# Optimization experiments

Measured on AMD Instinct MI355X. Metric: run time of the kernel, lower is better.

## Reference

```python
import jax, jax.numpy as jnp
import numpy as np

B, S, D, H, HD = 1, 4096, 1024, 16, 64
ROPE_THETA = 10000.0


def setup_inputs() -> dict:
    key = jax.random.key(0)
    ks = jax.random.split(key, 10)
    sc = 0.02
    hidden_states = jax.random.normal(ks[0], (B, S, D), dtype=jnp.float32)
    # sorted continuous timestamps in [0, S) (irregularly sampled time series)
    timestamps = jnp.sort(jax.random.uniform(ks[1], (B, S), dtype=jnp.float32), axis=-1) * S
    Wq = jax.random.normal(ks[2], (D, D), dtype=jnp.float32) * sc
    bq = jax.random.normal(ks[3], (D,), dtype=jnp.float32) * sc
    Wk = jax.random.normal(ks[4], (D, D), dtype=jnp.float32) * sc
    bk = jax.random.normal(ks[5], (D,), dtype=jnp.float32) * sc
    Wv = jax.random.normal(ks[6], (D, D), dtype=jnp.float32) * sc
    bv = jax.random.normal(ks[7], (D,), dtype=jnp.float32) * sc
    Wo = jax.random.normal(ks[8], (D, D), dtype=jnp.float32) * sc
    return dict(hidden_states=hidden_states, timestamps=timestamps,
                Wq=Wq, bq=bq, Wk=Wk, bk=bk, Wv=Wv, bv=bv, Wo=Wo)


def _rotate_half(x):
    x1, x2 = jnp.split(x, 2, axis=-1)
    return jnp.concatenate([-x2, x1], axis=-1)


def _ct_rope(q, k, timestamps):
    # q,k: [b,h,s,hd]; timestamps: [b,s] continuous positions
    inv_freq = 1.0 / (ROPE_THETA ** (jnp.arange(0, HD, 2, dtype=jnp.float32) / HD))
    angles = timestamps[:, None, :, None] * inv_freq  # [b,1,s,hd/2]
    angles = jnp.concatenate([angles, angles], axis=-1)  # [b,1,s,hd]
    cos, sin = jnp.cos(angles), jnp.sin(angles)
    q = q * cos + _rotate_half(q) * sin
    k = k * cos + _rotate_half(k) * sin
    return q, k


def reference(hidden_states, timestamps, Wq, bq, Wk, bk, Wv, bv, Wo):
    b, s, _ = hidden_states.shape
    # nn.Linear convention: y = x @ W.T + b
    q = (hidden_states @ Wq.T + bq).reshape(b, s, H, HD).transpose(0, 2, 1, 3)
    k = (hidden_states @ Wk.T + bk).reshape(b, s, H, HD).transpose(0, 2, 1, 3)
    v = (hidden_states @ Wv.T + bv).reshape(b, s, H, HD).transpose(0, 2, 1, 3)
    q, k = _ct_rope(q, k, timestamps)
    scores = jnp.einsum('bhqd,bhkd->bhqk', q, k) / jnp.sqrt(jnp.float32(HD))
    # causal additive mask (built as in HF Qwen2Model)
    causal = jnp.tril(jnp.ones((s, s), dtype=bool))
    neg = jnp.finfo(jnp.float32).min
    scores = jnp.where(causal[None, None], scores, neg)
    attn = jax.nn.softmax(scores.astype(jnp.float32), axis=-1).astype(q.dtype)
    out = jnp.einsum('bhqk,bhkd->bhqd', attn, v)
    out = out.transpose(0, 2, 1, 3).reshape(b, s, H * HD)
    return out @ Wo.T
```

## Files before the change

kernel.cpp:

```cpp
#include <hip/hip_runtime.h>

#define S_LEN  4096
#define DMODEL 1024
#define NHEAD  16
#define HDIM   64

typedef float    f32x4  __attribute__((ext_vector_type(4)));
typedef float    f32x16 __attribute__((ext_vector_type(16)));
typedef _Float16 f16x8  __attribute__((ext_vector_type(8)));
typedef _Float16 f16x4v __attribute__((ext_vector_type(4)));
typedef __fp16   fp16x2 __attribute__((ext_vector_type(2)));
typedef unsigned int u32;
typedef u32 u32x4 __attribute__((ext_vector_type(4)));

__device__ __forceinline__ void gl2lds16(const _Float16* g, _Float16* l) {
  __builtin_amdgcn_global_load_lds(
      (const __attribute__((address_space(1))) unsigned int*)g,
      (__attribute__((address_space(3))) unsigned int*)l, 16, 0, 0);
}

__device__ __forceinline__ u32 pkrtz_u(float a, float b) {
  fp16x2 h = __builtin_amdgcn_cvt_pkrtz(a, b);
  return __builtin_bit_cast(u32, h);
}

__device__ __forceinline__ float m3(float a, float b, float c) {
  return fmaxf(fmaxf(a, b), c);
}

__global__ void cast_f32_f16_k(const float* __restrict__ in,
                               _Float16* __restrict__ out, int n) {
  int i = (blockIdx.x * blockDim.x + threadIdx.x) * 4;
  if (i + 3 < n) {
    const float4 v = *(const float4*)(in + i);
    f16x4v o = { (_Float16)v.x, (_Float16)v.y, (_Float16)v.z, (_Float16)v.w };
    *(f16x4v*)(out + i) = o;
  }
}

__global__ void cast4_k(const float* __restrict__ a, const float* __restrict__ b,
                        const float* __restrict__ c, const float* __restrict__ d,
                        _Float16* __restrict__ oa, _Float16* __restrict__ ob,
                        _Float16* __restrict__ oc, _Float16* __restrict__ od) {
  const int seg = blockIdx.y;
  const float* in = seg == 0 ? a : seg == 1 ? b : seg == 2 ? c : d;
  _Float16*   out = seg == 0 ? oa : seg == 1 ? ob : seg == 2 ? oc : od;
  const int i = (blockIdx.x * blockDim.x + threadIdx.x) * 4;
  const float4 v = *(const float4*)(in + i);
  f16x4v o = { (_Float16)v.x, (_Float16)v.y, (_Float16)v.z, (_Float16)v.w };
  *(f16x4v*)(out + i) = o;
}

__global__ __launch_bounds__(256)
void gemm_qkv(const _Float16* __restrict__ A,
              const _Float16* __restrict__ Bw,
              const float* __restrict__ bq,
              const float* __restrict__ bk,
              const float* __restrict__ bv,
              const float* __restrict__ ts,
              _Float16* __restrict__ Qb,
              _Float16* __restrict__ Kb,
              _Float16* __restrict__ Vtb)
{
  __shared__ _Float16 lA[128 * 64];
  __shared__ _Float16 lB[128 * 64];

  const int tid  = threadIdx.x;
  const int wid  = tid >> 6;
  const int lane = tid & 63;
  const int l16  = lane & 15;
  const int lg   = lane >> 4;
  const int wr = wid >> 1, wc = wid & 1;
  const int m0 = blockIdx.y * 128, n0 = blockIdx.x * 128;
  const int K = DMODEL, M = S_LEN;

  const int lrow   = lane >> 3;
  const int gchunk = (lane & 7) ^ lrow;

  f32x4 acc[4][4] = {};

  for (int k0 = 0; k0 < K; k0 += 64) {
#pragma unroll
    for (int it = 0; it < 4; ++it) {
      const int rbase = (it * 4 + wid) * 8;
      gl2lds16(A  + (size_t)(m0 + rbase + lrow) * K + k0 + gchunk * 8, &lA[rbase * 64]);
      gl2lds16(Bw + (size_t)(n0 + rbase + lrow) * K + k0 + gchunk * 8, &lB[rbase * 64]);
    }
    __syncthreads();
#pragma unroll
    for (int kk = 0; kk < 2; ++kk) {
      f16x8 af[4], bfr[4];
#pragma unroll
      for (int mr = 0; mr < 4; ++mr) {
        const int row = wr * 64 + mr * 16 + l16;
        const int ch  = (kk * 4 + lg) ^ (l16 & 7);
        af[mr] = *(const f16x8*)&lA[row * 64 + ch * 8];
      }
#pragma unroll
      for (int nr = 0; nr < 4; ++nr) {
        const int row = wc * 64 + nr * 16 + l16;
        const int ch  = (kk * 4 + lg) ^ (l16 & 7);
        bfr[nr] = *(const f16x8*)&lB[row * 64 + ch * 8];
      }
#pragma unroll
      for (int mr = 0; mr < 4; ++mr)
#pragma unroll
        for (int nr = 0; nr < 4; ++nr)
          acc[mr][nr] = __builtin_amdgcn_mfma_f32_16x16x32_f16(af[mr], bfr[nr], acc[mr][nr], 0, 0, 0);
    }
    __syncthreads();
  }

  if (n0 >= 2048) {
    const int dbase = n0 - 2048;
    float bvv[4];
#pragma unroll
    for (int nr = 0; nr < 4; ++nr) bvv[nr] = bv[dbase + wc * 64 + nr * 16 + l16];
#pragma unroll
    for (int mr = 0; mr < 4; ++mr) {
      const int mbase = m0 + wr * 64 + mr * 16 + lg * 4;
#pragma unroll
      for (int nr = 0; nr < 4; ++nr) {
        const int d = dbase + wc * 64 + nr * 16 + l16;
        f16x4v o = { (_Float16)(acc[mr][nr][0] + bvv[nr]),
                     (_Float16)(acc[mr][nr][1] + bvv[nr]),
                     (_Float16)(acc[mr][nr][2] + bvv[nr]),
                     (_Float16)(acc[mr][nr][3] + bvv[nr]) };
        *(f16x4v*)&Vtb[(size_t)d * M + mbase] = o;
      }
    }
  } else {
    _Float16* O = (n0 < 1024) ? Qb : Kb;
    const float* bias = (n0 < 1024) ? bq : bk;
    const int nloc = n0 & 1023;
    float bvv[4];
#pragma unroll
    for (int nr = 0; nr < 4; ++nr) bvv[nr] = bias[nloc + wc * 64 + nr * 16 + l16];
    const float L2T  = 13.287712379549449f / 32.0f;
    const float inv0 = exp2f(-(float)l16 * L2T);
    const float inv1 = exp2f(-(float)(l16 + 16) * L2T);
#pragma unroll
    for (int mr = 0; mr < 4; ++mr)
#pragma unroll
      for (int r = 0; r < 4; ++r) {
        const int m = m0 + wr * 64 + mr * 16 + lg * 4 + r;
        const float t = ts[m];
        float s0, c0, s1, c1;
        sincosf(t * inv0, &s0, &c0);
        sincosf(t * inv1, &s1, &c1);
        const float p0 = acc[mr][0][r] + bvv[0];
        const float p1 = acc[mr][1][r] + bvv[1];
        const float p2 = acc[mr][2][r] + bvv[2];
        const float p3 = acc[mr][3][r] + bvv[3];
        const size_t base = (size_t)m * DMODEL + nloc + wc * 64 + l16;
        O[base + 0 ] = (_Float16)(p0 * c0 - p2 * s0);
        O[base + 16] = (_Float16)(p1 * c1 - p3 * s1);
        O[base + 32] = (_Float16)(p2 * c0 + p0 * s0);
        O[base + 48] = (_Float16)(p3 * c1 + p1 * s1);
      }
  }
}

__global__ __launch_bounds__(256)
void gemm_o(const _Float16* __restrict__ A,
            const _Float16* __restrict__ Bw,
            float* __restrict__ O)
{
  __shared__ _Float16 lA[64 * 64];
  __shared__ _Float16 lB[128 * 64];

  const int tid  = threadIdx.x;
  const int wid  = tid >> 6;
  const int lane = tid & 63;
  const int l16  = lane & 15;
  const int lg   = lane >> 4;
  const int wr = wid >> 1, wc = wid & 1;
  const int m0 = blockIdx.y * 64, n0 = blockIdx.x * 128;
  const int K = DMODEL, N = DMODEL;

  const int lrow   = lane >> 3;
  const int gchunk = (lane & 7) ^ lrow;

  f32x4 acc[2][4] = {};

  for (int k0 = 0; k0 < K; k0 += 64) {
#pragma unroll
    for (int it = 0; it < 2; ++it) {
      const int rbase = (it * 4 + wid) * 8;
      gl2lds16(A + (size_t)(m0 + rbase + lrow) * K + k0 + gchunk * 8, &lA[rbase * 64]);
    }
#pragma unroll
    for (int it = 0; it < 4; ++it) {
      const int rbase = (it * 4 + wid) * 8;
      gl2lds16(Bw + (size_t)(n0 + rbase + lrow) * K + k0 + gchunk * 8, &lB[rbase * 64]);
    }
    __syncthreads();
#pragma unroll
    for (int kk = 0; kk < 2; ++kk) {
      f16x8 af[2], bfr[4];
#pragma unroll
      for (int mr = 0; mr < 2; ++mr) {
        const int row = wr * 32 + mr * 16 + l16;
        const int ch  = (kk * 4 + lg) ^ (l16 & 7);
        af[mr] = *(const f16x8*)&lA[row * 64 + ch * 8];
      }
#pragma unroll
      for (int nr = 0; nr < 4; ++nr) {
        const int row = wc * 64 + nr * 16 + l16;
        const int ch  = (kk * 4 + lg) ^ (l16 & 7);
        bfr[nr] = *(const f16x8*)&lB[row * 64 + ch * 8];
      }
#pragma unroll
      for (int mr = 0; mr < 2; ++mr)
#pragma unroll
        for (int nr = 0; nr < 4; ++nr)
          acc[mr][nr] = __builtin_amdgcn_mfma_f32_16x16x32_f16(af[mr], bfr[nr], acc[mr][nr], 0, 0, 0);
    }
    __syncthreads();
  }

#pragma unroll
  for (int mr = 0; mr < 2; ++mr)
#pragma unroll
    for (int r = 0; r < 4; ++r) {
      const int m = m0 + wr * 32 + mr * 16 + lg * 4 + r;
#pragma unroll
      for (int nr = 0; nr < 4; ++nr) {
        const int n = n0 + wc * 64 + nr * 16 + l16;
        O[(size_t)m * N + n] = acc[mr][nr][r];
      }
    }
}

__device__ __forceinline__ void stage_tiles(const _Float16* __restrict__ Km,
                                            const _Float16* __restrict__ Vt,
                                            _Float16* kdst, _Float16* vdst,
                                            int kv0, int h, int wid, int lane) {
#pragma unroll
  for (int j8 = 0; j8 < 2; ++j8) {
    const int rb  = wid * 16 + j8 * 8;
    const int row = rb + (lane >> 3);
    const int g   = (lane & 7) ^ (row & 7);
    gl2lds16(Km + (size_t)(kv0 + row) * DMODEL + h * HDIM + g * 8, kdst + rb * 64);
    gl2lds16(Vt + (size_t)(h * HDIM + row) * S_LEN + kv0 + g * 8, vdst + rb * 64);
  }
}

__device__ __forceinline__ int part_off(int jb) {
  if (jb >= 24) return 40 + (jb - 24) * 4;
  if (jb >= 16) return 16 + (jb - 16) * 3;
  return (jb - 8) * 2;
}

__global__ __launch_bounds__(256, 4)
void attn_fwd(const _Float16* __restrict__ Q,
              const _Float16* __restrict__ Km,
              const _Float16* __restrict__ Vt,
              _Float16* __restrict__ Om,
              _Float16* __restrict__ pO0,
              _Float16* __restrict__ pO1,
              float* __restrict__ ps)
{
  __shared__ __align__(16) _Float16 smem[2][2][64 * 64];

  const int tid  = threadIdx.x;
  const int wid  = tid >> 6, lane = tid & 63;
  const int l31  = lane & 31;
  const bool hi  = (lane & 32) != 0;
  const int flat = blockIdx.x, xcd = flat & 7, idx = flat >> 3;
  const int h    = xcd * 2 + (idx & 1);
  const int slot = idx >> 1;
  int jb, part, parts;
  if (slot < 32)      { jb = 31 - (slot >> 2);              part = slot & 3;  parts = 4; }
  else if (slot < 56) { const int t = slot - 32; jb = 23 - t / 3; part = t % 3; parts = 3; }
  else if (slot < 72) { const int t = slot - 56; jb = 15 - (t >> 1); part = t & 1; parts = 2; }
  else                { jb = 79 - slot;                     part = 0;        parts = 1; }
  const int nt  = 2 * jb + 2;
  const int kt0 = (nt * part) / parts, kt1 = (nt * (part + 1)) / parts;
  const bool partial = parts > 1;
  const int u = partial ? (h * 72 + part_off(jb) + part) : 0;
  const int q0w = jb * 128 + wid * 32;
  const int sw  = l31 & 7;

  f16x8 qf[4];
  {
    const float qs = 0.18033688f;
    const size_t qbase = (size_t)(q0w + l31) * DMODEL + h * HDIM + (hi ? 8 : 0);
#pragma unroll
    for (int ks = 0; ks < 4; ++ks) {
      f16x8 t = *(const f16x8*)&Q[qbase + ks * 16];
#pragma unroll
      for (int e = 0; e < 8; ++e) qf[ks][e] = (_Float16)((float)t[e] * qs);
    }
  }

  f32x16 acc0, acc1;
#pragma unroll
  for (int r = 0; r < 16; ++r) { acc0[r] = 0.f; acc1[r] = 0.f; }
  float m_run = 0.f, l_run = 0.f;

  stage_tiles(Km, Vt, &smem[0][0][0], &smem[0][1][0], kt0 * 64, h, wid, lane);
  __syncthreads();
  int cur = 0;

  for (int kt = kt0; kt < kt1; ++kt) {
    if (kt + 1 < kt1)
      stage_tiles(Km, Vt, &smem[cur ^ 1][0][0], &smem[cur ^ 1][1][0],
                  (kt + 1) * 64, h, wid, lane);

    const int kv0 = kt * 64;
    if (kv0 <= q0w + 31) {
      const _Float16* kb = &smem[cur][0][0];
      const _Float16* vb = &smem[cur][1][0];

      f32x16 s0, s1;
#pragma unroll
      for (int r = 0; r < 16; ++r) { s0[r] = -m_run; s1[r] = -m_run; }
      __builtin_amdgcn_s_setprio(1);
#pragma unroll
      for (int ks = 0; ks < 4; ++ks) {
        const int cs = ((ks * 2 + (hi ? 1 : 0)) ^ sw) * 8;
        const f16x8 ka0 = *(const f16x8*)&kb[l31 * 64 + cs];
        const f16x8 ka1 = *(const f16x8*)&kb[(32 + l31) * 64 + cs];
        s0 = __builtin_amdgcn_mfma_f32_32x32x16_f16(ka0, qf[ks], s0, 0, 0, 0);
        s1 = __builtin_amdgcn_mfma_f32_32x32x16_f16(ka1, qf[ks], s1, 0, 0, 0);
      }
      __builtin_amdgcn_s_setprio(0);

      if (kv0 + 63 > q0w) {
        const int q = q0w + l31;
#pragma unroll
        for (int r = 0; r < 16; ++r) {
          const int kvr = kv0 + (r & 3) + 8 * (r >> 2) + (hi ? 4 : 0);
          if (kvr > q)      s0[r] = -1e30f;
          if (kvr + 32 > q) s1[r] = -1e30f;
        }
      }

      float t10[10];
#pragma unroll
      for (int p = 0; p < 5; ++p) {
        t10[p]     = m3(s0[3*p], s0[3*p+1], s0[3*p+2]);
        t10[5 + p] = m3(s1[3*p], s1[3*p+1], s1[3*p+2]);
      }
      float u0 = m3(t10[0], t10[1], t10[2]);
      float u1 = m3(t10[3], t10[4], s0[15]);
      float u2 = m3(t10[5], t10[6], t10[7]);
      float u3 = m3(t10[8], t10[9], s1[15]);
      float pm = fmaxf(m3(u0, u1, u2), u3);
      pm = fmaxf(pm, __shfl_xor(pm, 32));

      if (!__all(pm <= 10.f)) {
        m_run += pm;
        const float scl = exp2f(-pm);
        l_run *= scl;
#pragma unroll
        for (int r = 0; r < 16; ++r) { acc0[r] *= scl; acc1[r] *= scl; }
#pragma unroll
        for (int r = 0; r < 16; ++r) { s0[r] -= pm; s1[r] -= pm; }
      }

      float sa = 0.f, sb = 0.f, sc = 0.f, sd = 0.f;
#pragma unroll
      for (int r = 0; r < 16; r += 2) {
        s0[r]   = exp2f(s0[r]);
        s0[r+1] = exp2f(s0[r+1]);
        s1[r]   = exp2f(s1[r]);
        s1[r+1] = exp2f(s1[r+1]);
        sa += s0[r]; sb += s0[r+1]; sc += s1[r]; sd += s1[r+1];
      }
      float rsum = (sa + sb) + (sc + sd);
      rsum += __shfl_xor(rsum, 32);
      l_run += rsum;

      u32 pk[2][8];
#pragma unroll
      for (int p = 0; p < 8; ++p) {
        pk[0][p] = pkrtz_u(s0[2*p], s0[2*p+1]);
        pk[1][p] = pkrtz_u(s1[2*p], s1[2*p+1]);
      }

      __builtin_amdgcn_s_setprio(1);
#pragma unroll
      for (int ks = 0; ks < 4; ++ks) {
        const int c = ks >> 1, base = (ks & 1) * 4;
        auto r0 = __builtin_amdgcn_permlane32_swap((int)pk[c][base + 0], (int)pk[c][base + 2], false, false);
        auto r1 = __builtin_amdgcn_permlane32_swap((int)pk[c][base + 1], (int)pk[c][base + 3], false, false);
        u32x4 bw;
        bw[0] = (u32)r0[0];
        bw[1] = (u32)r1[0];
        bw[2] = (u32)r0[1];
        bw[3] = (u32)r1[1];
        const f16x8 pb = __builtin_bit_cast(f16x8, bw);
        const int cs = ((ks * 2 + (hi ? 1 : 0)) ^ sw) * 8;
        const f16x8 va0 = *(const f16x8*)&vb[l31 * 64 + cs];
        const f16x8 va1 = *(const f16x8*)&vb[(32 + l31) * 64 + cs];
        acc0 = __builtin_amdgcn_mfma_f32_32x32x16_f16(va0, pb, acc0, 0, 0, 0);
        acc1 = __builtin_amdgcn_mfma_f32_32x32x16_f16(va1, pb, acc1, 0, 0, 0);
      }
      __builtin_amdgcn_s_setprio(0);
    }

    __syncthreads();
    cur ^= 1;
  }

  _Float16* tr = &smem[0][0][0] + wid * 2304;
  const float invl = 1.0f / l_run;
#pragma unroll
  for (int r = 0; r < 16; ++r) {
    const int d = (r & 3) + 8 * (r >> 2) + (hi ? 4 : 0);
    tr[l31 * 72 + d]      = (_Float16)(acc0[r] * invl);
    tr[l31 * 72 + 32 + d] = (_Float16)(acc1[r] * invl);
  }
  __syncthreads();
  if (partial) {
    if (!hi) ps[u * 128 + wid * 32 + l31] = m_run + log2f(l_run);
    _Float16* dst = (u < 832) ? (pO0 + (size_t)u * 8192)
                              : (pO1 + (size_t)(u - 832) * 8192);
#pragma unroll
    for (int cc = 0; cc < 4; ++cc) {
      const int qq = cc * 8 + (lane >> 3), c8 = lane & 7;
      const f16x8 v = *(const f16x8*)&tr[qq * 72 + c8 * 8];
      *(f16x8*)&dst[(wid * 32 + qq) * 64 + c8 * 8] = v;
    }
  } else {
#pragma unroll
    for (int cc = 0; cc < 4; ++cc) {
      const int qq = cc * 8 + (lane >> 3), c8 = lane & 7;
      const f16x8 v = *(const f16x8*)&tr[qq * 72 + c8 * 8];
      *(f16x8*)&Om[(size_t)(q0w + qq) * DMODEL + h * HDIM + c8 * 8] = v;
    }
  }
}

__global__ __launch_bounds__(256)
void combine_k(const _Float16* __restrict__ pO0,
               const _Float16* __restrict__ pO1,
               const float* __restrict__ ps,
               _Float16* __restrict__ Om)
{
  const int t  = blockIdx.x * 256 + threadIdx.x;
  const int d8 = t & 7;
  const int hh = (t >> 3) & 15;
  const int q  = 1024 + (t >> 7);
  const int j  = q >> 7;
  const int qr = q & 127;
  const int parts = (j >= 24) ? 4 : (j >= 16) ? 3 : 2;
  const int off   = (j >= 24) ? 40 + (j - 24) * 4
                  : (j >= 16) ? 16 + (j - 16) * 3
                  :             (j - 8) * 2;
  const int u0 = hh * 72 + off;

  float sv[4];
#pragma unroll
  for (int p = 0; p < 4; ++p)
    sv[p] = (p < parts) ? ps[(u0 + p) * 128 + qr] : -1e30f;
  const float S = fmaxf(fmaxf(sv[0], sv[1]), fmaxf(sv[2], sv[3]));

  float o[8] = {0.f, 0.f, 0.f, 0.f, 0.f, 0.f, 0.f, 0.f};
  float tot = 0.f;
#pragma unroll
  for (int p = 0; p < 4; ++p) {
    if (p < parts) {
      const float w = exp2f(sv[p] - S);
      tot += w;
      const int uu = u0 + p;
      const _Float16* pp = (uu < 832) ? (pO0 + (size_t)uu * 8192)
                                      : (pO1 + (size_t)(uu - 832) * 8192);
      const f16x8 v = *(const f16x8*)&pp[qr * 64 + d8 * 8];
#pragma unroll
      for (int e = 0; e < 8; ++e) o[e] += w * (float)v[e];
    }
  }
  const float inv = 1.0f / tot;
  f16x8 ov;
#pragma unroll
  for (int e = 0; e < 8; ++e) ov[e] = (_Float16)(o[e] * inv);
  *(f16x8*)&Om[(size_t)q * DMODEL + hh * 64 + d8 * 8] = ov;
}

extern "C" void kernel_launch(void* const* d_in, const int* in_sizes, int n_in,
                              void* d_out, int out_size, void* d_ws, size_t ws_size,
                              hipStream_t stream)
{
  const float* hs = (const float*)d_in[0];
  const float* ts = (const float*)d_in[1];
  const float* Wq = (const float*)d_in[2];
  const float* bq = (const float*)d_in[3];
  const float* Wk = (const float*)d_in[4];
  const float* bk = (const float*)d_in[5];
  const float* Wv = (const float*)d_in[6];
  const float* bv = (const float*)d_in[7];
  const float* Wo = (const float*)d_in[8];
  float* out = (float*)d_out;

  char* ws = (char*)d_ws;
  const size_t MB = 1024 * 1024;
  _Float16* hsb  = (_Float16*)(ws + 0 * MB);
  _Float16* wqb  = (_Float16*)(ws + 8 * MB);
  _Float16* wkb  = (_Float16*)(ws + 10 * MB);
  _Float16* wvb  = (_Float16*)(ws + 12 * MB);
  _Float16* wob  = (_Float16*)(ws + 14 * MB);
  _Float16* Qb   = (_Float16*)(ws + 16 * MB);
  _Float16* Kb   = (_Float16*)(ws + 24 * MB);
  _Float16* Vtb  = (_Float16*)(ws + 32 * MB);
  _Float16* attb = (_Float16*)(ws + 40 * MB);
  _Float16* pO0  = (_Float16*)(ws + 0 * MB);
  _Float16* pO1  = (_Float16*)d_out;
  float*    ps   = (float*)   (ws + (size_t)13631488);

  cast_f32_f16_k<<<dim3(4096), dim3(256), 0, stream>>>(hs, hsb, S_LEN * DMODEL);
  cast4_k<<<dim3(1024, 4), dim3(256), 0, stream>>>(Wq, Wk, Wv, Wo, wqb, wkb, wvb, wob);

  gemm_qkv<<<dim3(3072 / 128, S_LEN / 128), dim3(256), 0, stream>>>(
      hsb, wqb, bq, bk, bv, ts, Qb, Kb, Vtb);

  attn_fwd<<<dim3(1280), dim3(256), 0, stream>>>(Qb, Kb, Vtb, attb, pO0, pO1, ps);
  combine_k<<<dim3(1536), dim3(256), 0, stream>>>(pO0, pO1, ps, attb);

  gemm_o<<<dim3(DMODEL / 128, S_LEN / 64), dim3(256), 0, stream>>>(attb, wob, out);
}
```

Measured before the change: 152.6 us.

## Double attention block to 8 waves over 256 queries with table-driven split-KV

```diff
diff --git a/kernel.cpp b/kernel.cpp
--- a/kernel.cpp
+++ b/kernel.cpp
@@ -27,6 +27,21 @@
 __device__ __forceinline__ float m3(float a, float b, float c) {
   return fmaxf(fmaxf(a, b), c);
 }
+
+__device__ __constant__ unsigned char PARTS_OF[16] =
+  {1,1,1,2,2,2,3,3,4,4,4,5,5,5,6,6};
+__device__ __constant__ unsigned char OFF_OF[16] =
+  {0,0,0,0,2,4,6,9,12,16,20,24,29,34,39,45};
+__device__ __constant__ unsigned char JB_TAB[54] = {
+  2, 5,5, 13,13,13,13,13, 10,10,10,10, 7,7,7,
+  15,15,15,15,15,15, 12,12,12,12,12, 4,4, 9,9,9,9,
+  14,14,14,14,14,14, 11,11,11,11,11, 6,6,6, 8,8,8,8,
+  3,3, 1, 0};
+__device__ __constant__ unsigned char PT_TAB[54] = {
+  0, 0,1, 0,1,2,3,4, 0,1,2,3, 0,1,2,
+  0,1,2,3,4,5, 0,1,2,3,4, 0,1, 0,1,2,3,
+  0,1,2,3,4,5, 0,1,2,3,4, 0,1,2, 0,1,2,3,
+  0,1, 0, 0};
 
 __global__ void cast_f32_f16_k(const float* __restrict__ in,
                                _Float16* __restrict__ out, int n) {
@@ -236,23 +251,14 @@
                                             const _Float16* __restrict__ Vt,
                                             _Float16* kdst, _Float16* vdst,
                                             int kv0, int h, int wid, int lane) {
-#pragma unroll
-  for (int j8 = 0; j8 < 2; ++j8) {
-    const int rb  = wid * 16 + j8 * 8;
-    const int row = rb + (lane >> 3);
-    const int g   = (lane & 7) ^ (row & 7);
-    gl2lds16(Km + (size_t)(kv0 + row) * DMODEL + h * HDIM + g * 8, kdst + rb * 64);
-    gl2lds16(Vt + (size_t)(h * HDIM + row) * S_LEN + kv0 + g * 8, vdst + rb * 64);
-  }
-}
-
-__device__ __forceinline__ int part_off(int jb) {
-  if (jb >= 24) return 40 + (jb - 24) * 4;
-  if (jb >= 16) return 16 + (jb - 16) * 3;
-  return (jb - 8) * 2;
-}
-
-__global__ __launch_bounds__(256, 4)
+  const int rb  = wid * 8;
+  const int row = rb + (lane >> 3);
+  const int g   = (lane & 7) ^ (row & 7);
+  gl2lds16(Km + (size_t)(kv0 + row) * DMODEL + h * HDIM + g * 8, kdst + rb * 64);
+  gl2lds16(Vt + (size_t)(h * HDIM + row) * S_LEN + kv0 + g * 8, vdst + rb * 64);
+}
+
+__global__ __launch_bounds__(512, 8)
 void attn_fwd(const _Float16* __restrict__ Q,
               const _Float16* __restrict__ Km,
               const _Float16* __restrict__ Vt,
@@ -261,7 +267,7 @@
               _Float16* __restrict__ pO1,
               float* __restrict__ ps)
 {
-  __shared__ __align__(16) _Float16 smem[2][2][64 * 64];
+  __shared__ __align__(16) _Float16 smem[18432];
 
   const int tid  = threadIdx.x;
   const int wid  = tid >> 6, lane = tid & 63;
@@ -270,16 +276,14 @@
   const int flat = blockIdx.x, xcd = flat & 7, idx = flat >> 3;
   const int h    = xcd * 2 + (idx & 1);
   const int slot = idx >> 1;
-  int jb, part, parts;
-  if (slot < 32)      { jb = 31 - (slot >> 2);              part = slot & 3;  parts = 4; }
-  else if (slot < 56) { const int t = slot - 32; jb = 23 - t / 3; part = t % 3; parts = 3; }
-  else if (slot < 72) { const int t = slot - 56; jb = 15 - (t >> 1); part = t & 1; parts = 2; }
-  else                { jb = 79 - slot;                     part = 0;        parts = 1; }
-  const int nt  = 2 * jb + 2;
+  const int jb    = JB_TAB[slot];
+  const int part  = PT_TAB[slot];
+  const int parts = PARTS_OF[jb];
+  const int nt  = 4 * (jb + 1);
   const int kt0 = (nt * part) / parts, kt1 = (nt * (part + 1)) / parts;
   const bool partial = parts > 1;
-  const int u = partial ? (h * 72 + part_off(jb) + part) : 0;
-  const int q0w = jb * 128 + wid * 32;
+  const int u = partial ? (h * 51 + OFF_OF[jb] + part) : 0;
+  const int q0w = jb * 256 + wid * 32;
   const int sw  = l31 & 7;
 
   f16x8 qf[4];
@@ -299,19 +303,19 @@
   for (int r = 0; r < 16; ++r) { acc0[r] = 0.f; acc1[r] = 0.f; }
   float m_run = 0.f, l_run = 0.f;
 
-  stage_tiles(Km, Vt, &smem[0][0][0], &smem[0][1][0], kt0 * 64, h, wid, lane);
+  stage_tiles(Km, Vt, &smem[0], &smem[4096], kt0 * 64, h, wid, lane);
   __syncthreads();
   int cur = 0;
 
   for (int kt = kt0; kt < kt1; ++kt) {
     if (kt + 1 < kt1)
-      stage_tiles(Km, Vt, &smem[cur ^ 1][0][0], &smem[cur ^ 1][1][0],
+      stage_tiles(Km, Vt, &smem[(cur ^ 1) * 8192], &smem[(cur ^ 1) * 8192 + 4096],
                   (kt + 1) * 64, h, wid, lane);
 
     const int kv0 = kt * 64;
     if (kv0 <= q0w + 31) {
-      const _Float16* kb = &smem[cur][0][0];
-      const _Float16* vb = &smem[cur][1][0];
+      const _Float16* kb = &smem[cur * 8192];
+      const _Float16* vb = &smem[cur * 8192 + 4096];
 
       f32x16 s0, s1;
 #pragma unroll
@@ -405,7 +409,7 @@
     cur ^= 1;
   }
 
-  _Float16* tr = &smem[0][0][0] + wid * 2304;
+  _Float16* tr = &smem[0] + wid * 2304;
   const float invl = 1.0f / l_run;
 #pragma unroll
   for (int r = 0; r < 16; ++r) {
@@ -415,9 +419,9 @@
   }
   __syncthreads();
   if (partial) {
-    if (!hi) ps[u * 128 + wid * 32 + l31] = m_run + log2f(l_run);
-    _Float16* dst = (u < 832) ? (pO0 + (size_t)u * 8192)
-                              : (pO1 + (size_t)(u - 832) * 8192);
+    if (!hi) ps[u * 256 + wid * 32 + l31] = m_run + log2f(l_run);
+    _Float16* dst = (u < 416) ? (pO0 + (size_t)u * 16384)
+                              : (pO1 + (size_t)(u - 416) * 16384);
 #pragma unroll
     for (int cc = 0; cc < 4; ++cc) {
       const int qq = cc * 8 + (lane >> 3), c8 = lane & 7;
@@ -443,31 +447,28 @@
   const int t  = blockIdx.x * 256 + threadIdx.x;
   const int d8 = t & 7;
   const int hh = (t >> 3) & 15;
-  const int q  = 1024 + (t >> 7);
-  const int j  = q >> 7;
-  const int qr = q & 127;
-  const int parts = (j >= 24) ? 4 : (j >= 16) ? 3 : 2;
-  const int off   = (j >= 24) ? 40 + (j - 24) * 4
-                  : (j >= 16) ? 16 + (j - 16) * 3
-                  :             (j - 8) * 2;
-  const int u0 = hh * 72 + off;
-
-  float sv[4];
-#pragma unroll
-  for (int p = 0; p < 4; ++p)
-    sv[p] = (p < parts) ? ps[(u0 + p) * 128 + qr] : -1e30f;
-  const float S = fmaxf(fmaxf(sv[0], sv[1]), fmaxf(sv[2], sv[3]));
+  const int q  = 768 + (t >> 7);
+  const int j  = q >> 8;
+  const int qr = q & 255;
+  const int parts = PARTS_OF[j];
+  const int u0 = hh * 51 + OFF_OF[j];
+
+  float sv[6];
+#pragma unroll
+  for (int p = 0; p < 6; ++p)
+    sv[p] = (p < parts) ? ps[(u0 + p) * 256 + qr] : -1e30f;
+  const float S = fmaxf(m3(sv[0], sv[1], sv[2]), m3(sv[3], sv[4], sv[5]));
 
   float o[8] = {0.f, 0.f, 0.f, 0.f, 0.f, 0.f, 0.f, 0.f};
   float tot = 0.f;
 #pragma unroll
-  for (int p = 0; p < 4; ++p) {
+  for (int p = 0; p < 6; ++p) {
     if (p < parts) {
       const float w = exp2f(sv[p] - S);
       tot += w;
       const int uu = u0 + p;
-      const _Float16* pp = (uu < 832) ? (pO0 + (size_t)uu * 8192)
-                                      : (pO1 + (size_t)(uu - 832) * 8192);
+      const _Float16* pp = (uu < 416) ? (pO0 + (size_t)uu * 16384)
+                                      : (pO1 + (size_t)(uu - 416) * 16384);
       const f16x8 v = *(const f16x8*)&pp[qr * 64 + d8 * 8];
 #pragma unroll
       for (int e = 0; e < 8; ++e) o[e] += w * (float)v[e];
@@ -516,8 +517,8 @@
   gemm_qkv<<<dim3(3072 / 128, S_LEN / 128), dim3(256), 0, stream>>>(
       hsb, wqb, bq, bk, bv, ts, Qb, Kb, Vtb);
 
-  attn_fwd<<<dim3(1280), dim3(256), 0, stream>>>(Qb, Kb, Vtb, attb, pO0, pO1, ps);
-  combine_k<<<dim3(1536), dim3(256), 0, stream>>>(pO0, pO1, ps, attb);
+  attn_fwd<<<dim3(864), dim3(512), 0, stream>>>(Qb, Kb, Vtb, attb, pO0, pO1, ps);
+  combine_k<<<dim3(1664), dim3(256), 0, stream>>>(pO0, pO1, ps, attb);
 
   gemm_o<<<dim3(DMODEL / 128, S_LEN / 64), dim3(256), 0, stream>>>(attb, wob, out);
 }
```

New measurement: 407.0 us. +166.7%, slower.

## Merge cast kernels and remap GEMM blocks per XCD for L2 reuse

Applied to the files above, without the earlier changes.

```diff
diff --git a/kernel.cpp b/kernel.cpp
--- a/kernel.cpp
+++ b/kernel.cpp
@@ -28,24 +28,25 @@
   return fmaxf(fmaxf(a, b), c);
 }
 
-__global__ void cast_f32_f16_k(const float* __restrict__ in,
-                               _Float16* __restrict__ out, int n) {
-  int i = (blockIdx.x * blockDim.x + threadIdx.x) * 4;
-  if (i + 3 < n) {
-    const float4 v = *(const float4*)(in + i);
-    f16x4v o = { (_Float16)v.x, (_Float16)v.y, (_Float16)v.z, (_Float16)v.w };
-    *(f16x4v*)(out + i) = o;
-  }
-}
-
-__global__ void cast4_k(const float* __restrict__ a, const float* __restrict__ b,
-                        const float* __restrict__ c, const float* __restrict__ d,
-                        _Float16* __restrict__ oa, _Float16* __restrict__ ob,
-                        _Float16* __restrict__ oc, _Float16* __restrict__ od) {
-  const int seg = blockIdx.y;
-  const float* in = seg == 0 ? a : seg == 1 ? b : seg == 2 ? c : d;
-  _Float16*   out = seg == 0 ? oa : seg == 1 ? ob : seg == 2 ? oc : od;
-  const int i = (blockIdx.x * blockDim.x + threadIdx.x) * 4;
+__global__ void cast_all_k(const float* __restrict__ hs,
+                           const float* __restrict__ a, const float* __restrict__ b,
+                           const float* __restrict__ c, const float* __restrict__ d,
+                           _Float16* __restrict__ ohs,
+                           _Float16* __restrict__ oa, _Float16* __restrict__ ob,
+                           _Float16* __restrict__ oc, _Float16* __restrict__ od) {
+  const int bid = blockIdx.x;
+  const float* in;
+  _Float16* out;
+  int local;
+  if (bid < 4096) {
+    in = hs; out = ohs; local = bid;
+  } else {
+    const int seg = (bid - 4096) >> 10;
+    local = (bid - 4096) & 1023;
+    in  = seg == 0 ? a  : seg == 1 ? b  : seg == 2 ? c  : d;
+    out = seg == 0 ? oa : seg == 1 ? ob : seg == 2 ? oc : od;
+  }
+  const int i = (local * 256 + threadIdx.x) * 4;
   const float4 v = *(const float4*)(in + i);
   f16x4v o = { (_Float16)v.x, (_Float16)v.y, (_Float16)v.z, (_Float16)v.w };
   *(f16x4v*)(out + i) = o;
@@ -71,7 +72,9 @@
   const int l16  = lane & 15;
   const int lg   = lane >> 4;
   const int wr = wid >> 1, wc = wid & 1;
-  const int m0 = blockIdx.y * 128, n0 = blockIdx.x * 128;
+  const int bid = blockIdx.x, xcd = bid & 7, ci = bid >> 3;
+  const int n0 = (xcd * 3 + ci / 32) * 128;
+  const int m0 = (ci & 31) * 128;
   const int K = DMODEL, M = S_LEN;
 
   const int lrow   = lane >> 3;
@@ -175,7 +178,9 @@
   const int l16  = lane & 15;
   const int lg   = lane >> 4;
   const int wr = wid >> 1, wc = wid & 1;
-  const int m0 = blockIdx.y * 64, n0 = blockIdx.x * 128;
+  const int bid = blockIdx.x, xcd = bid & 7, ci = bid >> 3;
+  const int n0 = xcd * 128;
+  const int m0 = ci * 64;
   const int K = DMODEL, N = DMODEL;
 
   const int lrow   = lane >> 3;
@@ -510,14 +515,14 @@
   _Float16* pO1  = (_Float16*)d_out;
   float*    ps   = (float*)   (ws + (size_t)13631488);
 
-  cast_f32_f16_k<<<dim3(4096), dim3(256), 0, stream>>>(hs, hsb, S_LEN * DMODEL);
-  cast4_k<<<dim3(1024, 4), dim3(256), 0, stream>>>(Wq, Wk, Wv, Wo, wqb, wkb, wvb, wob);
-
-  gemm_qkv<<<dim3(3072 / 128, S_LEN / 128), dim3(256), 0, stream>>>(
+  cast_all_k<<<dim3(8192), dim3(256), 0, stream>>>(hs, Wq, Wk, Wv, Wo,
+                                                   hsb, wqb, wkb, wvb, wob);
+
+  gemm_qkv<<<dim3(768), dim3(256), 0, stream>>>(
       hsb, wqb, bq, bk, bv, ts, Qb, Kb, Vtb);
 
   attn_fwd<<<dim3(1280), dim3(256), 0, stream>>>(Qb, Kb, Vtb, attb, pO0, pO1, ps);
   combine_k<<<dim3(1536), dim3(256), 0, stream>>>(pO0, pO1, ps, attb);
 
-  gemm_o<<<dim3(DMODEL / 128, S_LEN / 64), dim3(256), 0, stream>>>(attb, wob, out);
-}
+  gemm_o<<<dim3(512), dim3(256), 0, stream>>>(attb, wob, out);
+}
```

Result: no change. 153.1 us (+0.4%).
